# Kernel tuning notes

Measured on AMD Instinct MI355X. Metric: run time of the kernel, lower is better.

## Reference

```python
import jax, jax.numpy as jnp
import numpy as np
from jax import lax

B, C_IN, N, C_OUT, K = 16, 128, 2048, 256, 20
EPS = 1e-5


def setup_inputs() -> dict:
    key = jax.random.key(0)
    k1, k2 = jax.random.split(key)
    x = jax.random.normal(k1, (B, C_IN, N), dtype=jnp.float32)
    W = jax.random.normal(k2, (C_OUT, 2 * C_IN), dtype=jnp.float32) * (1.0 / np.sqrt(2 * C_IN))
    gamma = jnp.ones((C_OUT,), dtype=jnp.float32)
    beta = jnp.zeros((C_OUT,), dtype=jnp.float32)
    return {"x": x, "W": W, "gamma": gamma, "beta": beta, "k": K}


def _knn_inds(x, k):
    # squared pairwise distance: (B, N, N); computed with no grad (stop_gradient)
    xs = lax.stop_gradient(x)
    inner = jnp.einsum('bcn,bcm->bnm', xs, xs)
    sq = jnp.sum(xs * xs, axis=1)  # (B, N)
    pd = sq[:, :, None] - 2.0 * inner + sq[:, None, :]
    _, inds = lax.top_k(-pd, k)  # smallest distances -> (B, N, k)
    return inds


def reference(x, W, gamma, beta, k):
    knn = _knn_inds(x, k)                                   # (B, N, k) int
    # gather neighbours: neigh[b,c,n,j] = x[b,c,knn[b,n,j]]
    neigh = jax.vmap(lambda xb, kb: xb[:, kb])(x, knn)      # (B, C, N, k)
    central = jnp.broadcast_to(x[:, :, :, None], neigh.shape)
    edge = jnp.concatenate([central, neigh - central], axis=1)  # (B, 2C, N, k)
    # 1x1 conv (bias-free) as GEMM
    y = jnp.einsum('oc,bcnk->bonk', W, edge)                # (B, C_out, N, k)
    # BatchNorm2d (training-mode batch stats) + affine
    mean = jnp.mean(y, axis=(0, 2, 3), keepdims=True)
    var = jnp.var(y, axis=(0, 2, 3), keepdims=True)
    y = (y - mean) * lax.rsqrt(var + EPS)
    y = y * gamma[None, :, None, None] + beta[None, :, None, None]
    y = jax.nn.relu(y)
    return jnp.max(y, axis=3)                               # (B, C_out, N)
```

## Files before the change

kernel.cpp:

```cpp
#include <hip/hip_runtime.h>

#define B_   16
#define CIN  128
#define NPT  2048
#define COUT 256
#define KNN  20
#define KEEP 16
#define CAND 64
#define SIFT 32
#define EPS  1e-5f
#define DBIAS 256.0f

#define SQ_OFF   0ull
#define IDX_OFF  131072ull
#define UT_OFF   2752512ull
#define VT_OFF   36306944ull
#define GS_OFF   69861376ull
#define ST_OFF   69865472ull
#define AMAX_OFF 69871616ull
#define AMIN_OFF 103426048ull
#define WS_NEED_FUSED 136980480ull
#define XT_OFF   UT_OFF
#define XHT_OFF  VT_OFF

typedef _Float16 f16x8 __attribute__((ext_vector_type(8)));
typedef float    f32x4 __attribute__((ext_vector_type(4)));
typedef float    f32x2 __attribute__((ext_vector_type(2)));

__global__ __launch_bounds__(256) void prep_kernel(const float* __restrict__ x,
                                                   float* __restrict__ xT,
                                                   _Float16* __restrict__ xhT,
                                                   float* __restrict__ sqh) {
    __shared__ float Ls[128 * 68];
    __shared__ float ps[4 * 64];
    const int b = blockIdx.y, n0 = blockIdx.x * 64, t = threadIdx.x;
    const float* xb = x + (size_t)b * CIN * NPT;
    #pragma unroll
    for (int e = 0; e < 8; ++e) {
        int f = e * 256 + t;
        int c = f >> 4, n4 = (f & 15) << 2;
        *(float4*)&Ls[c * 68 + n4] = *(const float4*)&xb[(size_t)c * NPT + n0 + n4];
    }
    __syncthreads();
    {
        int nl = t & 63, part = t >> 6;
        float acc = 0.f;
        #pragma unroll
        for (int j = 0; j < 32; ++j) {
            float vh = (float)(_Float16)Ls[(part * 32 + j) * 68 + nl];
            acc += vh * vh;
        }
        ps[part * 64 + nl] = acc;
    }
    #pragma unroll
    for (int e = 0; e < 2; ++e) {
        int u = e * 256 + t;
        int nl = u >> 3, ck = (u & 7) << 4;
        float vv[16];
        #pragma unroll
        for (int j = 0; j < 16; ++j) vv[j] = Ls[(ck + j) * 68 + nl];
        size_t row = (size_t)b * NPT + n0 + nl;
        #pragma unroll
        for (int j = 0; j < 4; ++j) {
            float4 w = {vv[4 * j], vv[4 * j + 1], vv[4 * j + 2], vv[4 * j + 3]};
            *(float4*)&xT[row * CIN + ck + 4 * j] = w;
        }
        f16x8 h0, h1;
        #pragma unroll
        for (int j = 0; j < 8; ++j) { h0[j] = (_Float16)vv[j]; h1[j] = (_Float16)vv[8 + j]; }
        *(f16x8*)&xhT[row * CIN + ck] = h0;
        *(f16x8*)&xhT[row * CIN + ck + 8] = h1;
    }
    __syncthreads();
    if (t < 64) sqh[b * NPT + n0 + t] = ps[t] + ps[64 + t] + ps[128 + t] + ps[192 + t];
}

__global__ void wconv_kernel(const float* __restrict__ W,
                             _Float16* __restrict__ Wu,
                             _Float16* __restrict__ Wv) {
    int gid = blockIdx.x * 256 + threadIdx.x;
    int o = gid >> 7, c = gid & 127;
    float w1 = W[o * 256 + c], w2 = W[o * 256 + 128 + c];
    Wu[gid] = (_Float16)(w1 - w2);
    Wv[gid] = (_Float16)w2;
}

__device__ __forceinline__ void stage_pts(const _Float16* __restrict__ xhb,
                                          _Float16* buf, int base_n, int t) {
    const int l15 = t & 15, ks = t >> 6;
    const int quad = (t >> 4) & 3;
    const int c = ks * 32 + quad * 8;
    #pragma unroll
    for (int e = 0; e < 4; ++e) {
        const int n = base_n + e * 16 + l15;
        const _Float16* src = xhb + (size_t)n * CIN + c;
        _Float16* dst = buf + (size_t)(e * 256 + (t & 192)) * 8;
        __builtin_amdgcn_global_load_lds(
            (const __attribute__((address_space(1))) void*)src,
            (__attribute__((address_space(3))) void*)dst, 16, 0, 0);
    }
}

__device__ __forceinline__ void stage_tile16(const _Float16* __restrict__ srcl,
                                             _Float16* dsthalf) {
    #pragma unroll
    for (int e = 0; e < 4; ++e) {
        __builtin_amdgcn_global_load_lds(
            (const __attribute__((address_space(1))) void*)(srcl + e * 32),
            (__attribute__((address_space(3))) void*)(dsthalf + (size_t)e * 512),
            16, 0, 0);
    }
}

__global__ __launch_bounds__(256, 2) void knn_kernel(const _Float16* __restrict__ xhT,
                                                     const float* __restrict__ sqh,
                                                     int* __restrict__ surv_out) {
    __shared__ char smraw[59392];
    _Float16* bufA = (_Float16*)smraw;
    float*    sqm  = (float*)(smraw + 18432);

    const int b  = blockIdx.y;
    const int q0 = blockIdx.x * 64;
    const int t  = threadIdx.x;
    const int lane = t & 63, wv = t >> 6;
    const int l15 = lane & 15, quad = lane >> 4;
    const _Float16* xhb = xhT + (size_t)b * NPT * CIN;

    #pragma unroll
    for (int e = 0; e < 8; ++e)
        sqm[e * 256 + t] = sqh[b * NPT + e * 256 + t] + DBIAS;

    stage_pts(xhb, bufA, q0, t);
    __syncthreads();

    f16x8 af[4][4];
    #pragma unroll
    for (int qh = 0; qh < 4; ++qh)
        #pragma unroll
        for (int ks = 0; ks < 4; ++ks)
            af[qh][ks] = *(const f16x8*)(bufA + (size_t)((qh * 4 + ks) * 64 + lane) * 8);
    __syncthreads();

    _Float16* wbuf = (_Float16*)(smraw + 26624 + wv * 8192);
    float*    DtW  = (float*)(smraw + wv * 4608);
    const _Float16* srcl = xhb + (size_t)(wv * 16 + l15) * CIN + quad * 8;

    stage_tile16(srcl, wbuf);

    float bd[KEEP];
    #pragma unroll
    for (int i = 0; i < KEEP; ++i) bd[i] = 3.0e38f;

    #pragma unroll 1
    for (int ss = 0; ss < 32; ++ss) {
        const int mb = ss * 64 + wv * 16;
        asm volatile("s_waitcnt vmcnt(0)" ::: "memory");
        __builtin_amdgcn_sched_barrier(0);
        const _Float16* cur = wbuf + (ss & 1) * 2048;
        f16x8 bf[4];
        #pragma unroll
        for (int ks = 0; ks < 4; ++ks)
            bf[ks] = *(const f16x8*)(cur + ks * 512 + lane * 8);
        float sm_ = sqm[mb + l15];
        asm volatile("s_waitcnt lgkmcnt(0)" ::: "memory");
        __builtin_amdgcn_sched_barrier(0);
        if (ss < 31)
            stage_tile16(srcl + (size_t)(ss + 1) * 64 * CIN,
                         wbuf + ((ss + 1) & 1) * 2048);
        __builtin_amdgcn_sched_barrier(0);
        f32x4 acc[4];
        #pragma unroll
        for (int qh = 0; qh < 4; ++qh) acc[qh] = (f32x4){0.f, 0.f, 0.f, 0.f};
        #pragma unroll
        for (int ks = 0; ks < 4; ++ks)
            #pragma unroll
            for (int qh = 0; qh < 4; ++qh)
                acc[qh] = __builtin_amdgcn_mfma_f32_16x16x32_f16(af[qh][ks], bf[ks], acc[qh], 0, 0, 0);
        const unsigned om = (unsigned)(mb + l15);
        #pragma unroll
        for (int qh = 0; qh < 4; ++qh) {
            #pragma unroll
            for (int rg = 0; rg < 4; ++rg) {
                int q = qh * 16 + quad * 4 + rg;
                float d = sm_ - 2.f * acc[qh][rg];
                DtW[q * 18 + l15] = __uint_as_float((__float_as_uint(d) & 0xFFFFF800u) | om);
            }
        }
        float nk[16];
        {
            const float* myrow = DtW + lane * 18;
            #pragma unroll
            for (int p = 0; p < 8; ++p) {
                f32x2 v = *(const f32x2*)(myrow + 2 * p);
                nk[2 * p] = v[0]; nk[2 * p + 1] = v[1];
            }
        }
        #pragma unroll
        for (int kk = 2; kk <= 16; kk <<= 1) {
            #pragma unroll
            for (int j = kk >> 1; j > 0; j >>= 1) {
                #pragma unroll
                for (int i = 0; i < 16; ++i) {
                    int p = i ^ j;
                    if (p > i) {
                        float a = nk[i], c = nk[p];
                        float lo = fminf(a, c), hi = fmaxf(a, c);
                        if ((i & kk) == 0) { nk[i] = lo; nk[p] = hi; }
                        else               { nk[i] = hi; nk[p] = lo; }
                    }
                }
            }
        }
        #pragma unroll
        for (int i = 0; i < 16; ++i) bd[i] = fminf(bd[i], nk[15 - i]);
        #pragma unroll
        for (int j = 8; j > 0; j >>= 1) {
            #pragma unroll
            for (int i = 0; i < 16; ++i) {
                int p = i ^ j;
                if (p > i) {
                    float a = bd[i], c = bd[p];
                    bd[i] = fminf(a, c);
                    bd[p] = fmaxf(a, c);
                }
            }
        }
    }

    __syncthreads();

    float* Keys = (float*)smraw;
    #pragma unroll
    for (int i = 0; i < KEEP; ++i)
        Keys[lane * 65 + wv * KEEP + i] = bd[i];
    __syncthreads();
    {
        int cnt[KEEP];
        #pragma unroll
        for (int i = 0; i < KEEP; ++i) cnt[i] = 0;
        #pragma unroll 4
        for (int j = 0; j < CAND; ++j) {
            float kj = Keys[lane * 65 + j];
            #pragma unroll
            for (int i = 0; i < KEEP; ++i)
                cnt[i] += (kj < bd[i]) ? 1 : 0;
        }
        int* dst = surv_out + ((size_t)b * NPT + q0 + lane) * SIFT;
        #pragma unroll
        for (int i = 0; i < KEEP; ++i)
            if (cnt[i] < SIFT)
                dst[cnt[i]] = (int)(__float_as_uint(bd[i]) & 0x7FFu);
    }
}

__global__ __launch_bounds__(256, 4) void refine_kernel(const float* __restrict__ xT,
                                                        const int* __restrict__ surv,
                                                        int* __restrict__ knn_out) {
    __shared__ float  Qs[16 * 128];
    __shared__ int    sidx[16 * 32];
    __shared__ double ddL[16 * 32];
    const int b = blockIdx.y, q0 = blockIdx.x * 16, t = threadIdx.x;
    const float* xTb = xT + (size_t)b * NPT * CIN;
    #pragma unroll
    for (int e = 0; e < 2; ++e)
        sidx[e * 256 + t] = surv[((size_t)b * NPT + q0) * SIFT + e * 256 + t];
    #pragma unroll
    for (int e = 0; e < 2; ++e) {
        int f = e * 256 + t;
        int row = f >> 5, c4 = (f & 31) << 2;
        *(float4*)&Qs[row * 128 + c4] = *(const float4*)&xTb[(size_t)(q0 + row) * CIN + c4];
    }
    __syncthreads();
    const int g = t >> 3, j = t & 7;
    #pragma unroll 1
    for (int it = 0; it < 16; ++it) {
        int pair = it * 32 + g;
        int q = pair >> 5, k = pair & 31;
        int m = sidx[q * 32 + k];
        const float* mrow = xTb + (size_t)m * CIN + j * 16;
        const float* qrow = Qs + q * 128 + j * 16;
        float4 a0 = *(const float4*)&mrow[0];
        float4 a1 = *(const float4*)&mrow[4];
        float4 a2 = *(const float4*)&mrow[8];
        float4 a3 = *(const float4*)&mrow[12];
        float4 c0 = *(const float4*)&qrow[0];
        float4 c1 = *(const float4*)&qrow[4];
        float4 c2 = *(const float4*)&qrow[8];
        float4 c3 = *(const float4*)&qrow[12];
        double ss = 0.0, d0;
        d0 = (double)c0.x - (double)a0.x; ss = fma(d0, d0, ss);
        d0 = (double)c0.y - (double)a0.y; ss = fma(d0, d0, ss);
        d0 = (double)c0.z - (double)a0.z; ss = fma(d0, d0, ss);
        d0 = (double)c0.w - (double)a0.w; ss = fma(d0, d0, ss);
        d0 = (double)c1.x - (double)a1.x; ss = fma(d0, d0, ss);
        d0 = (double)c1.y - (double)a1.y; ss = fma(d0, d0, ss);
        d0 = (double)c1.z - (double)a1.z; ss = fma(d0, d0, ss);
        d0 = (double)c1.w - (double)a1.w; ss = fma(d0, d0, ss);
        d0 = (double)c2.x - (double)a2.x; ss = fma(d0, d0, ss);
        d0 = (double)c2.y - (double)a2.y; ss = fma(d0, d0, ss);
        d0 = (double)c2.z - (double)a2.z; ss = fma(d0, d0, ss);
        d0 = (double)c2.w - (double)a2.w; ss = fma(d0, d0, ss);
        d0 = (double)c3.x - (double)a3.x; ss = fma(d0, d0, ss);
        d0 = (double)c3.y - (double)a3.y; ss = fma(d0, d0, ss);
        d0 = (double)c3.z - (double)a3.z; ss = fma(d0, d0, ss);
        d0 = (double)c3.w - (double)a3.w; ss = fma(d0, d0, ss);
        ss += __shfl_xor(ss, 1, 8);
        ss += __shfl_xor(ss, 2, 8);
        ss += __shfl_xor(ss, 4, 8);
        if (j == 0) ddL[q * 32 + k] = ss;
    }
    __syncthreads();
    const int q = t >> 4, kk = (t & 15) << 1;
    int* dst = knn_out + ((size_t)b * NPT + q0 + q) * KNN;
    #pragma unroll
    for (int e = 0; e < 2; ++e) {
        int k = kk + e;
        double mine = ddL[q * 32 + k];
        int c = 0;
        #pragma unroll 4
        for (int jx = 0; jx < SIFT; ++jx)
            c += (ddL[q * 32 + jx] < mine) ? 1 : 0;
        if (c < KNN) dst[c] = sidx[q * 32 + k];
    }
}

__global__ __launch_bounds__(256, 2) void knn_kernel_fb(const _Float16* __restrict__ xhT,
                                                        const float* __restrict__ xT,
                                                        const float* __restrict__ sqh,
                                                        int* __restrict__ knn_out) {
    __shared__ char smraw[59392];
    _Float16* bufA = (_Float16*)smraw;
    float*    sqm  = (float*)(smraw + 18432);

    const int b  = blockIdx.y;
    const int q0 = blockIdx.x * 64;
    const int t  = threadIdx.x;
    const int lane = t & 63, wv = t >> 6;
    const int l15 = lane & 15, quad = lane >> 4;
    const _Float16* xhb = xhT + (size_t)b * NPT * CIN;

    #pragma unroll
    for (int e = 0; e < 8; ++e)
        sqm[e * 256 + t] = sqh[b * NPT + e * 256 + t] + DBIAS;

    stage_pts(xhb, bufA, q0, t);
    __syncthreads();

    f16x8 af[4][4];
    #pragma unroll
    for (int qh = 0; qh < 4; ++qh)
        #pragma unroll
        for (int ks = 0; ks < 4; ++ks)
            af[qh][ks] = *(const f16x8*)(bufA + (size_t)((qh * 4 + ks) * 64 + lane) * 8);
    __syncthreads();

    _Float16* wbuf = (_Float16*)(smraw + 26624 + wv * 8192);
    float*    DtW  = (float*)(smraw + wv * 4608);
    const _Float16* srcl = xhb + (size_t)(wv * 16 + l15) * CIN + quad * 8;
    stage_tile16(srcl, wbuf);

    float bd[KEEP];
    #pragma unroll
    for (int i = 0; i < KEEP; ++i) bd[i] = 3.0e38f;

    #pragma unroll 1
    for (int ss = 0; ss < 32; ++ss) {
        const int mb = ss * 64 + wv * 16;
        asm volatile("s_waitcnt vmcnt(0)" ::: "memory");
        __builtin_amdgcn_sched_barrier(0);
        const _Float16* cur = wbuf + (ss & 1) * 2048;
        f16x8 bf[4];
        #pragma unroll
        for (int ks = 0; ks < 4; ++ks)
            bf[ks] = *(const f16x8*)(cur + ks * 512 + lane * 8);
        float sm_ = sqm[mb + l15];
        asm volatile("s_waitcnt lgkmcnt(0)" ::: "memory");
        __builtin_amdgcn_sched_barrier(0);
        if (ss < 31)
            stage_tile16(srcl + (size_t)(ss + 1) * 64 * CIN,
                         wbuf + ((ss + 1) & 1) * 2048);
        __builtin_amdgcn_sched_barrier(0);
        f32x4 acc[4];
        #pragma unroll
        for (int qh = 0; qh < 4; ++qh) acc[qh] = (f32x4){0.f, 0.f, 0.f, 0.f};
        #pragma unroll
        for (int ks = 0; ks < 4; ++ks)
            #pragma unroll
            for (int qh = 0; qh < 4; ++qh)
                acc[qh] = __builtin_amdgcn_mfma_f32_16x16x32_f16(af[qh][ks], bf[ks], acc[qh], 0, 0, 0);
        const unsigned om = (unsigned)(mb + l15);
        #pragma unroll
        for (int qh = 0; qh < 4; ++qh) {
            #pragma unroll
            for (int rg = 0; rg < 4; ++rg) {
                int q = qh * 16 + quad * 4 + rg;
                float d = sm_ - 2.f * acc[qh][rg];
                DtW[q * 18 + l15] = __uint_as_float((__float_as_uint(d) & 0xFFFFF800u) | om);
            }
        }
        float nk[16];
        {
            const float* myrow = DtW + lane * 18;
            #pragma unroll
            for (int p = 0; p < 8; ++p) {
                f32x2 v = *(const f32x2*)(myrow + 2 * p);
                nk[2 * p] = v[0]; nk[2 * p + 1] = v[1];
            }
        }
        #pragma unroll
        for (int kk = 2; kk <= 16; kk <<= 1) {
            #pragma unroll
            for (int j = kk >> 1; j > 0; j >>= 1) {
                #pragma unroll
                for (int i = 0; i < 16; ++i) {
                    int p = i ^ j;
                    if (p > i) {
                        float a = nk[i], c = nk[p];
                        float lo = fminf(a, c), hi = fmaxf(a, c);
                        if ((i & kk) == 0) { nk[i] = lo; nk[p] = hi; }
                        else               { nk[i] = hi; nk[p] = lo; }
                    }
                }
            }
        }
        #pragma unroll
        for (int i = 0; i < 16; ++i) bd[i] = fminf(bd[i], nk[15 - i]);
        #pragma unroll
        for (int j = 8; j > 0; j >>= 1) {
            #pragma unroll
            for (int i = 0; i < 16; ++i) {
                int p = i ^ j;
                if (p > i) {
                    float a = bd[i], c = bd[p];
                    bd[i] = fminf(a, c);
                    bd[p] = fmaxf(a, c);
                }
            }
        }
    }

    __syncthreads();

    float*  Keys = (float*)smraw;
    int*    Surv = (int*)(smraw + 16640);
    double* ddL  = (double*)(smraw + 25088);
    #pragma unroll
    for (int i = 0; i < KEEP; ++i)
        Keys[lane * 65 + wv * KEEP + i] = bd[i];
    __syncthreads();
    {
        int cnt[KEEP];
        #pragma unroll
        for (int i = 0; i < KEEP; ++i) cnt[i] = 0;
        #pragma unroll 4
        for (int j = 0; j < CAND; ++j) {
            float kj = Keys[lane * 65 + j];
            #pragma unroll
            for (int i = 0; i < KEEP; ++i)
                cnt[i] += (kj < bd[i]) ? 1 : 0;
        }
        __syncthreads();
        #pragma unroll
        for (int i = 0; i < KEEP; ++i)
            if (cnt[i] < SIFT)
                Surv[lane * 33 + cnt[i]] = (int)(__float_as_uint(bd[i]) & 0x7FFu);
    }
    __syncthreads();

    int ms[8];
    #pragma unroll
    for (int k = 0; k < 8; ++k) ms[k] = Surv[lane * 33 + wv * 8 + k] & 2047;
    double dd8[8];
    #pragma unroll
    for (int k = 0; k < 8; ++k) dd8[k] = 0.0;
    const float* xTb = xT + (size_t)b * NPT * CIN;
    const float* qrow = xTb + (size_t)(q0 + lane) * CIN;
    #pragma unroll 1
    for (int ch = 0; ch < 8; ++ch) {
        double qd[16];
        #pragma unroll
        for (int j = 0; j < 4; ++j) {
            float4 qv = *(const float4*)&qrow[ch * 16 + 4 * j];
            qd[4 * j] = (double)qv.x; qd[4 * j + 1] = (double)qv.y;
            qd[4 * j + 2] = (double)qv.z; qd[4 * j + 3] = (double)qv.w;
        }
        #pragma unroll
        for (int k = 0; k < 8; ++k) {
            const float* mrow = xTb + (size_t)ms[k] * CIN + ch * 16;
            float4 ma = *(const float4*)&mrow[0];
            float4 mb2 = *(const float4*)&mrow[4];
            float4 mc = *(const float4*)&mrow[8];
            float4 md = *(const float4*)&mrow[12];
            double ss = dd8[k], d0;
            d0 = qd[0]  - (double)ma.x;  ss = fma(d0, d0, ss);
            d0 = qd[1]  - (double)ma.y;  ss = fma(d0, d0, ss);
            d0 = qd[2]  - (double)ma.z;  ss = fma(d0, d0, ss);
            d0 = qd[3]  - (double)ma.w;  ss = fma(d0, d0, ss);
            d0 = qd[4]  - (double)mb2.x; ss = fma(d0, d0, ss);
            d0 = qd[5]  - (double)mb2.y; ss = fma(d0, d0, ss);
            d0 = qd[6]  - (double)mb2.z; ss = fma(d0, d0, ss);
            d0 = qd[7]  - (double)mb2.w; ss = fma(d0, d0, ss);
            d0 = qd[8]  - (double)mc.x;  ss = fma(d0, d0, ss);
            d0 = qd[9]  - (double)mc.y;  ss = fma(d0, d0, ss);
            d0 = qd[10] - (double)mc.z;  ss = fma(d0, d0, ss);
            d0 = qd[11] - (double)mc.w;  ss = fma(d0, d0, ss);
            d0 = qd[12] - (double)md.x;  ss = fma(d0, d0, ss);
            d0 = qd[13] - (double)md.y;  ss = fma(d0, d0, ss);
            d0 = qd[14] - (double)md.z;  ss = fma(d0, d0, ss);
            d0 = qd[15] - (double)md.w;  ss = fma(d0, d0, ss);
            dd8[k] = ss;
        }
    }
    #pragma unroll
    for (int k = 0; k < 8; ++k) ddL[lane * 33 + wv * 8 + k] = dd8[k];
    __syncthreads();
    int* dst = knn_out + ((size_t)b * NPT + q0 + lane) * KNN;
    #pragma unroll
    for (int k = 0; k < 8; ++k) {
        int c = 0;
        #pragma unroll 4
        for (int j = 0; j < SIFT; ++j)
            c += (ddL[lane * 33 + j] < dd8[k]) ? 1 : 0;
        if (c < KNN) dst[c] = ms[k];
    }
}

__global__ __launch_bounds__(256) void uv_gemm_h(const _Float16* __restrict__ xhT,
                                                 const _Float16* __restrict__ Wu,
                                                 const _Float16* __restrict__ Wv,
                                                 float* __restrict__ uT,
                                                 float* __restrict__ vT) {
    __shared__ _Float16 Bx[8192];
    const int b = blockIdx.y, n0 = blockIdx.x * 64, t = threadIdx.x;
    const int lane = t & 63, w = t >> 6, l15 = lane & 15, quad = lane >> 4;
    stage_pts(xhT + (size_t)b * NPT * CIN, Bx, n0, t);
    __syncthreads();
    f16x8 bf[4];
    #pragma unroll
    for (int ks = 0; ks < 4; ++ks)
        bf[ks] = *(const f16x8*)(Bx + (size_t)((w * 4 + ks) * 64 + lane) * 8);
    const int n = n0 + w * 16 + l15;
    #pragma unroll 1
    for (int ot = 0; ot < 16; ++ot) {
        const _Float16* wu = Wu + (size_t)(ot * 16 + l15) * 128 + quad * 8;
        const _Float16* wv2 = Wv + (size_t)(ot * 16 + l15) * 128 + quad * 8;
        f32x4 au = (f32x4){0.f, 0.f, 0.f, 0.f};
        f32x4 av = (f32x4){0.f, 0.f, 0.f, 0.f};
        #pragma unroll
        for (int ks = 0; ks < 4; ++ks) {
            f16x8 a_u = *(const f16x8*)(wu + ks * 32);
            f16x8 a_v = *(const f16x8*)(wv2 + ks * 32);
            au = __builtin_amdgcn_mfma_f32_16x16x32_f16(a_u, bf[ks], au, 0, 0, 0);
            av = __builtin_amdgcn_mfma_f32_16x16x32_f16(a_v, bf[ks], av, 0, 0, 0);
        }
        size_t base = ((size_t)b * NPT + n) * COUT + ot * 16 + quad * 4;
        *(f32x4*)&uT[base] = au;
        *(f32x4*)&vT[base] = av;
    }
}

__global__ __launch_bounds__(256) void uv_gemm(const float* __restrict__ x,
                                               const float* __restrict__ W,
                                               float* __restrict__ uT,
                                               float* __restrict__ vT) {
    __shared__ float Ax[32 * 64];
    __shared__ float Bu[32 * 68];
    __shared__ float Bv[32 * 68];
    const int b  = blockIdx.z;
    const int n0 = blockIdx.x * 64;
    const int o0 = blockIdx.y * 64;
    const int t  = threadIdx.x;
    const int tx = t & 15, ty = t >> 4;
    const float* xb = x + (size_t)b * CIN * NPT;
    float au[4][4], av_[4][4];
    #pragma unroll
    for (int i = 0; i < 4; ++i)
        #pragma unroll
        for (int j = 0; j < 4; ++j) { au[i][j] = 0.f; av_[i][j] = 0.f; }
    #pragma unroll 1
    for (int kc = 0; kc < 4; ++kc) {
        const int c0 = kc * 32;
        __syncthreads();
        #pragma unroll
        for (int e = 0; e < 2; ++e) {
            int f = e * 256 + t;
            int cz = f >> 4, ni = (f & 15) << 2;
            *(float4*)&Ax[(cz << 6) + ni] = *(const float4*)&xb[(size_t)(c0 + cz) * NPT + n0 + ni];
        }
        #pragma unroll
        for (int e = 0; e < 8; ++e) {
            int ii = e * 256 + t;
            int cz = ii & 31, oj = ii >> 5;
            float w1 = W[(size_t)(o0 + oj) * 256 + c0 + cz];
            float w2 = W[(size_t)(o0 + oj) * 256 + 128 + c0 + cz];
            Bu[cz * 68 + oj] = w1 - w2;
            Bv[cz * 68 + oj] = w2;
        }
        __syncthreads();
        #pragma unroll 8
        for (int cz = 0; cz < 32; ++cz) {
            const float4 a4 = *(const float4*)&Ax[(cz << 6) + (tx << 2)];
            float bu0 = Bu[cz * 68 + (ty << 2) + 0], bv0 = Bv[cz * 68 + (ty << 2) + 0];
            float bu1 = Bu[cz * 68 + (ty << 2) + 1], bv1 = Bv[cz * 68 + (ty << 2) + 1];
            float bu2 = Bu[cz * 68 + (ty << 2) + 2], bv2 = Bv[cz * 68 + (ty << 2) + 2];
            float bu3 = Bu[cz * 68 + (ty << 2) + 3], bv3 = Bv[cz * 68 + (ty << 2) + 3];
            au[0][0] += a4.x * bu0; au[0][1] += a4.x * bu1; au[0][2] += a4.x * bu2; au[0][3] += a4.x * bu3;
            au[1][0] += a4.y * bu0; au[1][1] += a4.y * bu1; au[1][2] += a4.y * bu2; au[1][3] += a4.y * bu3;
            au[2][0] += a4.z * bu0; au[2][1] += a4.z * bu1; au[2][2] += a4.z * bu2; au[2][3] += a4.z * bu3;
            au[3][0] += a4.w * bu0; au[3][1] += a4.w * bu1; au[3][2] += a4.w * bu2; au[3][3] += a4.w * bu3;
            av_[0][0] += a4.x * bv0; av_[0][1] += a4.x * bv1; av_[0][2] += a4.x * bv2; av_[0][3] += a4.x * bv3;
            av_[1][0] += a4.y * bv0; av_[1][1] += a4.y * bv1; av_[1][2] += a4.y * bv2; av_[1][3] += a4.y * bv3;
            av_[2][0] += a4.z * bv0; av_[2][1] += a4.z * bv1; av_[2][2] += a4.z * bv2; av_[2][3] += a4.z * bv3;
            av_[3][0] += a4.w * bv0; av_[3][1] += a4.w * bv1; av_[3][2] += a4.w * bv2; av_[3][3] += a4.w * bv3;
        }
    }
    #pragma unroll
    for (int i = 0; i < 4; ++i) {
        int n = n0 + (tx << 2) + i;
        size_t base = ((size_t)b * NPT + n) * COUT + o0 + (ty << 2);
        float4 u4 = {au[i][0], au[i][1], au[i][2], au[i][3]};
        float4 v4 = {av_[i][0], av_[i][1], av_[i][2], av_[i][3]};
        *(float4*)&uT[base] = u4;
        *(float4*)&vT[base] = v4;
    }
}

__global__ __launch_bounds__(256) void gather_stats(const float* __restrict__ uT,
                                                    const float* __restrict__ vT,
                                                    const int* __restrict__ knn_in,
                                                    double* __restrict__ gsum,
                                                    float* __restrict__ aMax,
                                                    float* __restrict__ aMin) {
    __shared__ int sidx[16 * KNN];
    const int b  = blockIdx.y;
    const int n0 = blockIdx.x * 64 + blockIdx.z * 16;
    const int o  = threadIdx.x;
    for (int e = o; e < 16 * KNN; e += 256)
        sidx[e] = knn_in[((size_t)b * NPT + n0) * KNN + e];
    __syncthreads();
    const float* ub = uT + ((size_t)b * NPT + n0) * COUT + o;
    const float* vb = vT + (size_t)b * NPT * COUT + o;
    float* amx = aMax + ((size_t)b * NPT + n0) * COUT + o;
    float* amn = aMin + ((size_t)b * NPT + n0) * COUT + o;
    double s1 = 0.0, s2 = 0.0;
    #pragma unroll 1
    for (int s = 0; s < 16; ++s) {
        float u = ub[(size_t)s * COUT];
        float vmax = -3e38f, vmin = 3e38f, vsum = 0.f, vsq = 0.f;
        #pragma unroll
        for (int j = 0; j < KNN; ++j) {
            float v = vb[(size_t)sidx[s * KNN + j] * COUT];
            vmax = fmaxf(vmax, v);
            vmin = fminf(vmin, v);
            vsum += v;
            vsq = fmaf(v, v, vsq);
        }
        s1 += 20.0 * (double)u + (double)vsum;
        s2 += 20.0 * (double)u * (double)u + 2.0 * (double)u * (double)vsum + (double)vsq;
        amx[(size_t)s * COUT] = vmax;
        amn[(size_t)s * COUT] = vmin;
    }
    atomicAdd(&gsum[o], s1);
    atomicAdd(&gsum[COUT + o], s2);
}

__global__ __launch_bounds__(256) void stats_kernel(const float* __restrict__ uT,
                                                    const float* __restrict__ vT,
                                                    const int* __restrict__ knn_in,
                                                    double* __restrict__ gsum) {
    __shared__ int sidx[64 * KNN];
    const int b  = blockIdx.y;
    const int n0 = blockIdx.x * 64;
    const int o  = threadIdx.x;
    for (int e = o; e < 64 * KNN; e += 256)
        sidx[e] = knn_in[((size_t)b * NPT + n0) * KNN + e];
    __syncthreads();
    const float* ub = uT + ((size_t)b * NPT + n0) * COUT + o;
    const float* vb = vT + (size_t)b * NPT * COUT + o;
    double s1 = 0.0, s2 = 0.0;
    #pragma unroll 1
    for (int s = 0; s < 64; ++s) {
        float u = ub[(size_t)s * COUT];
        #pragma unroll
        for (int j = 0; j < KNN; ++j) {
            float y = u + vb[(size_t)sidx[s * KNN + j] * COUT];
            s1 += (double)y;
            s2 = fma((double)y, (double)y, s2);
        }
    }
    atomicAdd(&gsum[o], s1);
    atomicAdd(&gsum[COUT + o], s2);
}

__global__ void finalize_kernel(const double* __restrict__ gsum,
                                const float* __restrict__ gamma,
                                const float* __restrict__ beta,
                                float* __restrict__ st) {
    const int o = threadIdx.x;
    const double M = (double)B_ * NPT * KNN;
    double mean = gsum[o] / M;
    double var  = gsum[COUT + o] / M - mean * mean;
    float inv = 1.0f / sqrtf((float)var + EPS);
    float s = gamma[o] * inv;
    st[o] = s;
    st[COUT + o] = beta[o] - (float)mean * s;
}

__global__ __launch_bounds__(256, 2) void out2_kernel(const float* __restrict__ uT,
                                                      const float* __restrict__ aMax,
                                                      const float* __restrict__ aMin,
                                                      const float* __restrict__ st,
                                                      float* __restrict__ out) {
    __shared__ float zt[256 * 68];
    const int b  = blockIdx.y;
    const int n0 = blockIdx.x * 64;
    const int o  = threadIdx.x;
    const float s  = st[o];
    const float tt = st[COUT + o];
    const float* ub  = uT   + ((size_t)b * NPT + n0) * COUT + o;
    const float* amx = aMax + ((size_t)b * NPT + n0) * COUT + o;
    const float* amn = aMin + ((size_t)b * NPT + n0) * COUT + o;
    #pragma unroll 2
    for (int si = 0; si < 64; ++si) {
        float u = ub[(size_t)si * COUT];
        float y1 = u + amx[(size_t)si * COUT];
        float y2 = u + amn[(size_t)si * COUT];
        float z1 = fmaxf(s * y1 + tt, 0.f);
        float z2 = fmaxf(s * y2 + tt, 0.f);
        zt[o * 68 + si] = fmaxf(z1, z2);
    }
    __syncthreads();
    float* dst = out + ((size_t)b * COUT + o) * NPT + n0;
    #pragma unroll
    for (int i = 0; i < 16; ++i)
        *(float4*)&dst[i * 4] = *(const float4*)&zt[o * 68 + i * 4];
}

__global__ __launch_bounds__(256, 2) void out_kernel(const float* __restrict__ uT,
                                                     const float* __restrict__ vT,
                                                     const int* __restrict__ knn_in,
                                                     const float* __restrict__ st,
                                                     float* __restrict__ out) {
    __shared__ int sidx[64 * KNN];
    __shared__ float zt[256 * 68];
    const int b  = blockIdx.y;
    const int n0 = blockIdx.x * 64;
    const int o  = threadIdx.x;
    for (int e = o; e < 64 * KNN; e += 256)
        sidx[e] = knn_in[((size_t)b * NPT + n0) * KNN + e];
    __syncthreads();
    const float s  = st[o];
    const float tt = st[COUT + o];
    const float* ub = uT + ((size_t)b * NPT + n0) * COUT + o;
    const float* vb = vT + (size_t)b * NPT * COUT + o;
    #pragma unroll 1
    for (int si = 0; si < 64; ++si) {
        float u = ub[(size_t)si * COUT];
        float ymax = -3e38f, ymin = 3e38f;
        #pragma unroll
        for (int j = 0; j < KNN; ++j) {
            float y = u + vb[(size_t)sidx[si * KNN + j] * COUT];
            ymax = fmaxf(ymax, y);
            ymin = fminf(ymin, y);
        }
        float z1 = fmaxf(s * ymax + tt, 0.f);
        float z2 = fmaxf(s * ymin + tt, 0.f);
        zt[o * 68 + si] = fmaxf(z1, z2);
    }
    __syncthreads();
    float* dst = out + ((size_t)b * COUT + o) * NPT + n0;
    #pragma unroll
    for (int i = 0; i < 16; ++i)
        *(float4*)&dst[i * 4] = *(const float4*)&zt[o * 68 + i * 4];
}

extern "C" void kernel_launch(void* const* d_in, const int* in_sizes, int n_in,
                              void* d_out, int out_size, void* d_ws, size_t ws_size,
                              hipStream_t stream) {
    const float* x     = (const float*)d_in[0];
    const float* W     = (const float*)d_in[1];
    const float* gamma = (const float*)d_in[2];
    const float* beta  = (const float*)d_in[3];
    float* out = (float*)d_out;
    char* ws = (char*)d_ws;
    float*     sqh  = (float*)(ws + SQ_OFF);
    int*       idx  = (int*)(ws + IDX_OFF);
    float*     uT   = (float*)(ws + UT_OFF);
    float*     vT   = (float*)(ws + VT_OFF);
    double*    gsum = (double*)(ws + GS_OFF);
    float*     st   = (float*)(ws + ST_OFF);
    float*     aMax = (float*)(ws + AMAX_OFF);
    float*     aMin = (float*)(ws + AMIN_OFF);
    const bool fused = (ws_size >= WS_NEED_FUSED);

    hipMemsetAsync(gsum, 0, 2 * COUT * sizeof(double), stream);
    if (fused) {
        float*    xT  = (float*)(ws + AMAX_OFF);
        _Float16* xhT = (_Float16*)(ws + AMAX_OFF + 16777216ull);
        _Float16* Wu  = (_Float16*)(ws + AMAX_OFF + 25165824ull);
        _Float16* Wv  = (_Float16*)(ws + AMAX_OFF + 25231360ull);
        int*      svG = (int*)(ws + UT_OFF);
        prep_kernel<<<dim3(32, 16), 256, 0, stream>>>(x, xT, xhT, sqh);
        wconv_kernel<<<128, 256, 0, stream>>>(W, Wu, Wv);
        knn_kernel<<<dim3(32, 16), 256, 0, stream>>>(xhT, sqh, svG);
        refine_kernel<<<dim3(128, 16), 256, 0, stream>>>(xT, svG, idx);
        uv_gemm_h<<<dim3(32, 16), 256, 0, stream>>>(xhT, Wu, Wv, uT, vT);
        gather_stats<<<dim3(32, 16, 4), 256, 0, stream>>>(uT, vT, idx, gsum, aMax, aMin);
        finalize_kernel<<<1, 256, 0, stream>>>(gsum, gamma, beta, st);
        out2_kernel<<<dim3(32, 16), 256, 0, stream>>>(uT, aMax, aMin, st, out);
    } else {
        float*    xT  = (float*)(ws + XT_OFF);
        _Float16* xhT = (_Float16*)(ws + XHT_OFF);
        prep_kernel<<<dim3(32, 16), 256, 0, stream>>>(x, xT, xhT, sqh);
        knn_kernel_fb<<<dim3(32, 16), 256, 0, stream>>>(xhT, xT, sqh, idx);
        uv_gemm<<<dim3(32, 4, 16), 256, 0, stream>>>(x, W, uT, vT);
        stats_kernel<<<dim3(32, 16), 256, 0, stream>>>(uT, vT, idx, gsum);
        finalize_kernel<<<1, 256, 0, stream>>>(gsum, gamma, beta, st);
        out_kernel<<<dim3(32, 16), 256, 0, stream>>>(uT, vT, idx, st, out);
    }
}
```

Before: 336.8 us.

## Remap blocks so each XCD owns one batch and fold u into gathered extrema

The knn, refine and gather_stats kernels now use a flat 1D grid whose block id is decoded so that consecutive ids go round-robin to XCDs, keeping each batch's data on one XCD's L2. gather_stats writes u+vmax and u+vmin with nontemporal stores, so out2_kernel no longer reads uT and loads one fewer stream per element. This aims to cut L2 misses across XCDs and HBM traffic in the epilogue. It relies on the hardware dispatching blocks round-robin across 8 XCDs.

```diff
diff --git a/kernel.cpp b/kernel.cpp
--- a/kernel.cpp
+++ b/kernel.cpp
@@ -119,8 +119,10 @@
     _Float16* bufA = (_Float16*)smraw;
     float*    sqm  = (float*)(smraw + 18432);
 
-    const int b  = blockIdx.y;
-    const int q0 = blockIdx.x * 64;
+    const int id  = blockIdx.x;
+    const int xcd = id & 7, qq = id >> 3;
+    const int b   = xcd + ((qq >> 5) << 3);
+    const int q0  = (qq & 31) * 64;
     const int t  = threadIdx.x;
     const int lane = t & 63, wv = t >> 6;
     const int l15 = lane & 15, quad = lane >> 4;
@@ -259,7 +261,11 @@
     __shared__ float  Qs[16 * 128];
     __shared__ int    sidx[16 * 32];
     __shared__ double ddL[16 * 32];
-    const int b = blockIdx.y, q0 = blockIdx.x * 16, t = threadIdx.x;
+    const int id  = blockIdx.x;
+    const int xcd = id & 7, qq = id >> 3;
+    const int b   = xcd + ((qq >> 7) << 3);
+    const int q0  = (qq & 127) * 16;
+    const int t = threadIdx.x;
     const float* xTb = xT + (size_t)b * NPT * CIN;
     #pragma unroll
     for (int e = 0; e < 2; ++e)
@@ -632,9 +638,12 @@
                                                     float* __restrict__ aMax,
                                                     float* __restrict__ aMin) {
     __shared__ int sidx[16 * KNN];
-    const int b  = blockIdx.y;
-    const int n0 = blockIdx.x * 64 + blockIdx.z * 16;
-    const int o  = threadIdx.x;
+    const int id  = blockIdx.x;
+    const int xcd = id & 7, qq = id >> 3;
+    const int b   = xcd + ((qq >> 7) << 3);
+    const int inner = qq & 127;
+    const int n0  = (inner >> 2) * 64 + (inner & 3) * 16;
+    const int o   = threadIdx.x;
     for (int e = o; e < 16 * KNN; e += 256)
         sidx[e] = knn_in[((size_t)b * NPT + n0) * KNN + e];
     __syncthreads();
@@ -657,8 +666,10 @@
         }
         s1 += 20.0 * (double)u + (double)vsum;
         s2 += 20.0 * (double)u * (double)u + 2.0 * (double)u * (double)vsum + (double)vsq;
-        amx[(size_t)s * COUT] = vmax;
-        amn[(size_t)s * COUT] = vmin;
+        float y1 = u + vmax;
+        float y2 = u + vmin;
+        __builtin_nontemporal_store(y1, &amx[(size_t)s * COUT]);
+        __builtin_nontemporal_store(y2, &amn[(size_t)s * COUT]);
     }
     atomicAdd(&gsum[o], s1);
     atomicAdd(&gsum[COUT + o], s2);
@@ -706,8 +717,7 @@
     st[COUT + o] = beta[o] - (float)mean * s;
 }
 
-__global__ __launch_bounds__(256, 2) void out2_kernel(const float* __restrict__ uT,
-                                                      const float* __restrict__ aMax,
+__global__ __launch_bounds__(256, 2) void out2_kernel(const float* __restrict__ aMax,
                                                       const float* __restrict__ aMin,
                                                       const float* __restrict__ st,
                                                       float* __restrict__ out) {
@@ -717,14 +727,12 @@
     const int o  = threadIdx.x;
     const float s  = st[o];
     const float tt = st[COUT + o];
-    const float* ub  = uT   + ((size_t)b * NPT + n0) * COUT + o;
     const float* amx = aMax + ((size_t)b * NPT + n0) * COUT + o;
     const float* amn = aMin + ((size_t)b * NPT + n0) * COUT + o;
     #pragma unroll 2
     for (int si = 0; si < 64; ++si) {
-        float u = ub[(size_t)si * COUT];
-        float y1 = u + amx[(size_t)si * COUT];
-        float y2 = u + amn[(size_t)si * COUT];
+        float y1 = amx[(size_t)si * COUT];
+        float y2 = amn[(size_t)si * COUT];
         float z1 = fmaxf(s * y1 + tt, 0.f);
         float z2 = fmaxf(s * y2 + tt, 0.f);
         zt[o * 68 + si] = fmaxf(z1, z2);
@@ -802,12 +810,12 @@
         int*      svG = (int*)(ws + UT_OFF);
         prep_kernel<<<dim3(32, 16), 256, 0, stream>>>(x, xT, xhT, sqh);
         wconv_kernel<<<128, 256, 0, stream>>>(W, Wu, Wv);
-        knn_kernel<<<dim3(32, 16), 256, 0, stream>>>(xhT, sqh, svG);
-        refine_kernel<<<dim3(128, 16), 256, 0, stream>>>(xT, svG, idx);
+        knn_kernel<<<512, 256, 0, stream>>>(xhT, sqh, svG);
+        refine_kernel<<<2048, 256, 0, stream>>>(xT, svG, idx);
         uv_gemm_h<<<dim3(32, 16), 256, 0, stream>>>(xhT, Wu, Wv, uT, vT);
-        gather_stats<<<dim3(32, 16, 4), 256, 0, stream>>>(uT, vT, idx, gsum, aMax, aMin);
+        gather_stats<<<2048, 256, 0, stream>>>(uT, vT, idx, gsum, aMax, aMin);
         finalize_kernel<<<1, 256, 0, stream>>>(gsum, gamma, beta, st);
-        out2_kernel<<<dim3(32, 16), 256, 0, stream>>>(uT, aMax, aMin, st, out);
+        out2_kernel<<<dim3(32, 16), 256, 0, stream>>>(aMax, aMin, st, out);
     } else {
         float*    xT  = (float*)(ws + XT_OFF);
         _Float16* xhT = (_Float16*)(ws + XHT_OFF);
```

Measured after the change: 307.6 us. -8.7%, faster.
